# Performance work log

Hardware: AMD Instinct MI355X
Metric: run time of the kernel (lower is better)

The kernel has to match this reference:

```python
import jax, jax.numpy as jnp
import numpy as np

N = 50000        # nodes
E = 1_600_000    # edges
F = 128          # dataset_num_features (== dim so layer weights stack)
D = 128          # hidden_dim
L = 3            # num_gc_layers
G = 512          # graphs in batch
BN_EPS = 1e-5


def setup_inputs() -> dict:
    key = jax.random.key(0)
    ks = jax.random.split(key, 12)
    s = 0.05
    x = jax.random.normal(ks[0], (N, F), jnp.float32)
    edge_index = jax.random.randint(ks[1], (2, E), 0, N)
    batch = jnp.sort(jax.random.randint(ks[2], (N,), 0, G))
    # GIN MLP per layer: Linear(F->D), ReLU, Linear(D->D)  (F==D so stackable)
    W1 = jax.random.normal(ks[3], (L, F, D), jnp.float32) * s
    b1 = jnp.zeros((L, D), jnp.float32)
    W2 = jax.random.normal(ks[4], (L, D, D), jnp.float32) * s
    b2 = jnp.zeros((L, D), jnp.float32)
    bn_gamma = jnp.ones((L, D), jnp.float32)
    bn_beta = jnp.zeros((L, D), jnp.float32)
    # proj_head: Linear(3D->3D), ReLU, Linear(3D->3D)
    ED = L * D
    Wp1 = jax.random.normal(ks[5], (ED, ED), jnp.float32) * s
    bp1 = jnp.zeros((ED,), jnp.float32)
    Wp2 = jax.random.normal(ks[6], (ED, ED), jnp.float32) * s
    bp2 = jnp.zeros((ED,), jnp.float32)
    return {"x": x, "edge_index": edge_index, "batch": batch,
            "W1": W1, "b1": b1, "W2": W2, "b2": b2,
            "bn_gamma": bn_gamma, "bn_beta": bn_beta,
            "Wp1": Wp1, "bp1": bp1, "Wp2": Wp2, "bp2": bp2}


def reference(x, edge_index, batch, W1, b1, W2, b2, bn_gamma, bn_beta, Wp1, bp1, Wp2, bp2):
    src, dst = edge_index[0], edge_index[1]
    h = x
    xs = []
    for i in range(L):
        # GINConv (eps=0): nn(x_i + sum_{j->i} x_j) via gather + scatter-add
        agg = jax.ops.segment_sum(h[src], dst, num_segments=N)  # [N, D]
        m = agg + h
        m = jax.nn.relu(m @ W1[i] + b1[i])
        m = m @ W2[i] + b2[i]
        m = jax.nn.relu(m)                 # outer F.relu in Encoder.forward
        # BatchNorm1d (training mode, biased variance)
        mu = m.mean(axis=0)
        var = m.var(axis=0)
        h = (m - mu) * jax.lax.rsqrt(var + BN_EPS) * bn_gamma[i] + bn_beta[i]
        xs.append(h)
    node = jnp.concatenate(xs, axis=1)                    # [N, L*D]
    pooled = jax.ops.segment_sum(node, batch, num_segments=G)  # global_add_pool [G, L*D]
    z = jax.nn.relu(pooled @ Wp1 + bp1) @ Wp2 + bp2       # proj_head
    return z
```

## Files before the change

### kernel.cpp

```cpp
#include <hip/hip_runtime.h>

#define NN 50000
#define NPAD 50048
#define NE 1600000
#define GG 512
#define PAD 96
#define NBKT 196
#define BCAP 12288
#define CHUNK 6250
#define NBLK_MLP 782
#define NRED1 196
#define BN_EPS 1e-5f

typedef __attribute__((ext_vector_type(8))) short short8;
typedef __attribute__((ext_vector_type(4))) float f32x4;

__device__ __forceinline__ unsigned short f2bf(float x) {
    unsigned int u = __builtin_bit_cast(unsigned int, x);
    return (unsigned short)((u + 0x7FFFu + ((u >> 16) & 1u)) >> 16);
}
__device__ __forceinline__ float bf2f(unsigned int b) {
    return __builtin_bit_cast(float, b << 16);
}

__global__ __launch_bounds__(256) void bucket_k(const int* __restrict__ src, const int* __restrict__ dst,
                                                int* __restrict__ bcur, unsigned int* __restrict__ staging) {
    __shared__ int hist[NBKT];
    __shared__ int curs[NBKT];
    const int t = threadIdx.x;
    if (t < NBKT) hist[t] = 0;
    __syncthreads();
    const int e0 = blockIdx.x * CHUNK;
    const int e1 = e0 + CHUNK;
    for (int e = e0 + t; e < e1; e += 256) atomicAdd(&hist[dst[e] >> 8], 1);
    __syncthreads();
    if (t < NBKT) {
        int c = hist[t];
        curs[t] = (c > 0) ? atomicAdd(&bcur[t], c) : 0;
    }
    __syncthreads();
    for (int e = e0 + t; e < e1; e += 256) {
        int d = dst[e];
        int b = d >> 8;
        int pos = atomicAdd(&curs[b], 1);
        staging[(size_t)b * BCAP + pos] = (unsigned int)(d & 255) | ((unsigned int)src[e] << 8);
    }
}

__global__ __launch_bounds__(256) void ellfill_k(const int* __restrict__ bcur,
                                                 const unsigned int* __restrict__ staging,
                                                 int* __restrict__ cnt, unsigned short* __restrict__ ell) {
    __shared__ unsigned short lell[256 * PAD];
    __shared__ int lcnt[256];
    const int b = blockIdx.x, t = threadIdx.x;
    lcnt[t] = 0;
    __syncthreads();
    const int tot = bcur[b];
    const unsigned int* sg = staging + (size_t)b * BCAP;
    for (int i = t; i < tot; i += 256) {
        unsigned int v = sg[i];
        int r = v & 255;
        int p = atomicAdd(&lcnt[r], 1);
        lell[r * PAD + p] = (unsigned short)(v >> 8);
    }
    __syncthreads();
    const int n0 = b << 8;
    const int nrows = min(256, NN - n0);
    for (int i = t; i < nrows * 12; i += 256) {
        int r = i / 12, q = i % 12;
        *(uint4*)(ell + (size_t)(n0 + r) * PAD + q * 8) = *(const uint4*)(lell + r * PAD + q * 8);
    }
    if (t < nrows) cnt[n0 + t] = lcnt[t];
}

__global__ __launch_bounds__(256) void xconv_k(const float* __restrict__ x, unsigned short* __restrict__ xb) {
    int i = blockIdx.x * 256 + threadIdx.x;
    const int tot = NN * 32;
    const int stp = gridDim.x * 256;
    for (; i < tot; i += stp) {
        float4 v = ((const float4*)x)[i];
        uint2 pk;
        pk.x = (unsigned int)f2bf(v.x) | ((unsigned int)f2bf(v.y) << 16);
        pk.y = (unsigned int)f2bf(v.z) | ((unsigned int)f2bf(v.w) << 16);
        ((uint2*)xb)[i] = pk;
    }
}

__global__ __launch_bounds__(256) void wconv_k(const float* __restrict__ W1, const float* __restrict__ W2,
                                               unsigned short* __restrict__ Wt) {
    int i = blockIdx.x * 256 + threadIdx.x;
    if (i >= 6 * 16384) return;
    int mat = i >> 14, rem = i & 16383;
    int c = rem >> 7, k = rem & 127;
    const float* Wsrc = (mat & 1) ? W2 : W1;
    int l = mat >> 1;
    float v = Wsrc[(size_t)l * 16384 + k * 128 + c];
    Wt[(size_t)mat * 16384 + c * 128 + k] = f2bf(v);
}

__global__ __launch_bounds__(256) void wpconv_k(const float* __restrict__ Wp1, const float* __restrict__ Wp2,
                                                unsigned short* __restrict__ Wpt) {
    int i = blockIdx.x * 256 + threadIdx.x;
    if (i >= 2 * 147456) return;
    int mat = i / 147456, rem = i % 147456;
    int c = rem / 384, k = rem % 384;
    const float* Wsrc = mat ? Wp2 : Wp1;
    Wpt[(size_t)mat * 147456 + c * 384 + k] = f2bf(Wsrc[(size_t)k * 384 + c]);
}

__global__ __launch_bounds__(256) void pconv_k(const float* __restrict__ p, unsigned short* __restrict__ pb) {
    int i = blockIdx.x * 256 + threadIdx.x;
    if (i >= GG * 384 / 4) return;
    float4 v = ((const float4*)p)[i];
    uint2 pk;
    pk.x = (unsigned int)f2bf(v.x) | ((unsigned int)f2bf(v.y) << 16);
    pk.y = (unsigned int)f2bf(v.z) | ((unsigned int)f2bf(v.w) << 16);
    ((uint2*)pb)[i] = pk;
}

__global__ __launch_bounds__(256) void agg_k(const int* __restrict__ cnt, const unsigned short* __restrict__ ell,
                                             const unsigned short* __restrict__ h, const float* __restrict__ ss,
                                             unsigned short* __restrict__ m) {
    int gid = blockIdx.x * 256 + threadIdx.x;
    int n = gid >> 4, l = gid & 15;
    if (n >= NN) return;
    float sc[8], sh[8];
    #pragma unroll
    for (int j = 0; j < 8; ++j) { sc[j] = 1.f; sh[j] = 0.f; }
    if (ss) {
        #pragma unroll
        for (int j = 0; j < 8; ++j) { sc[j] = ss[l * 8 + j]; sh[j] = ss[128 + l * 8 + j]; }
    }
    int e = cnt[n];
    const unsigned short* row = ell + (size_t)n * PAD;
    float acc[8];
    {
        uint4 q = *(const uint4*)(h + (size_t)n * 128 + l * 8);
        unsigned int qq[4] = {q.x, q.y, q.z, q.w};
        #pragma unroll
        for (int j = 0; j < 4; ++j) {
            acc[2 * j]     = bf2f(qq[j] & 0xffffu) * sc[2 * j];
            acc[2 * j + 1] = bf2f(qq[j] >> 16)     * sc[2 * j + 1];
        }
    }
    int i = 0;
    for (; i + 4 <= e; i += 4) {
        uint2 ip = *(const uint2*)(row + i);
        int s0 = ip.x & 0xffff, s1 = ip.x >> 16, s2 = ip.y & 0xffff, s3 = ip.y >> 16;
        uint4 q0 = *(const uint4*)(h + (size_t)s0 * 128 + l * 8);
        uint4 q1 = *(const uint4*)(h + (size_t)s1 * 128 + l * 8);
        uint4 q2 = *(const uint4*)(h + (size_t)s2 * 128 + l * 8);
        uint4 q3 = *(const uint4*)(h + (size_t)s3 * 128 + l * 8);
        unsigned int a0[4] = {q0.x, q0.y, q0.z, q0.w};
        unsigned int a1[4] = {q1.x, q1.y, q1.z, q1.w};
        unsigned int a2[4] = {q2.x, q2.y, q2.z, q2.w};
        unsigned int a3[4] = {q3.x, q3.y, q3.z, q3.w};
        #pragma unroll
        for (int j = 0; j < 4; ++j) {
            acc[2*j]   = fmaf(bf2f(a0[j] & 0xffffu), sc[2*j],
                         fmaf(bf2f(a1[j] & 0xffffu), sc[2*j],
                         fmaf(bf2f(a2[j] & 0xffffu), sc[2*j],
                         fmaf(bf2f(a3[j] & 0xffffu), sc[2*j], acc[2*j]))));
            acc[2*j+1] = fmaf(bf2f(a0[j] >> 16), sc[2*j+1],
                         fmaf(bf2f(a1[j] >> 16), sc[2*j+1],
                         fmaf(bf2f(a2[j] >> 16), sc[2*j+1],
                         fmaf(bf2f(a3[j] >> 16), sc[2*j+1], acc[2*j+1]))));
        }
    }
    for (; i < e; ++i) {
        int s0 = row[i];
        uint4 q = *(const uint4*)(h + (size_t)s0 * 128 + l * 8);
        unsigned int qq[4] = {q.x, q.y, q.z, q.w};
        #pragma unroll
        for (int j = 0; j < 4; ++j) {
            acc[2*j]   = fmaf(bf2f(qq[j] & 0xffffu), sc[2*j],   acc[2*j]);
            acc[2*j+1] = fmaf(bf2f(qq[j] >> 16),     sc[2*j+1], acc[2*j+1]);
        }
    }
    float fe = (float)(e + 1);
    #pragma unroll
    for (int j = 0; j < 8; ++j) acc[j] = fmaf(fe, sh[j], acc[j]);
    uint4 pk;
    pk.x = (unsigned int)f2bf(acc[0]) | ((unsigned int)f2bf(acc[1]) << 16);
    pk.y = (unsigned int)f2bf(acc[2]) | ((unsigned int)f2bf(acc[3]) << 16);
    pk.z = (unsigned int)f2bf(acc[4]) | ((unsigned int)f2bf(acc[5]) << 16);
    pk.w = (unsigned int)f2bf(acc[6]) | ((unsigned int)f2bf(acc[7]) << 16);
    *(uint4*)(m + (size_t)n * 128 + l * 8) = pk;
}

__global__ __launch_bounds__(256) void mlp_k(const unsigned short* __restrict__ A,
                                             const unsigned short* __restrict__ Wt,
                                             const float* __restrict__ bias1,
                                             const float* __restrict__ bias2,
                                             unsigned short* __restrict__ yb,
                                             float* __restrict__ scr) {
    __shared__ __align__(16) unsigned short sW[128 * 136];
    __shared__ __align__(16) unsigned short sT[64 * 136];
    float* sred = (float*)sT;
    const int tid = threadIdx.x;
    for (int ch = tid; ch < 2048; ch += 256) {
        int c = ch >> 4, i = ch & 15;
        *(uint4*)(sW + c * 136 + i * 8) = *(const uint4*)(Wt + c * 128 + i * 8);
    }
    const int w = tid >> 6, l = tid & 63;
    const int lr = l & 15, lk = l >> 4;
    const int row0 = blockIdx.x * 64 + w * 16;
    const unsigned short* ap = A + (size_t)(row0 + lr) * 128 + lk * 8;
    short8 af0 = *(const short8*)(ap);
    short8 af1 = *(const short8*)(ap + 32);
    short8 af2 = *(const short8*)(ap + 64);
    short8 af3 = *(const short8*)(ap + 96);
    f32x4 acc[8] = {};
    __syncthreads();
    #pragma unroll
    for (int c = 0; c < 8; ++c) {
        const unsigned short* wp = sW + (c * 16 + lr) * 136 + lk * 8;
        short8 wf0 = *(const short8*)(wp);
        short8 wf1 = *(const short8*)(wp + 32);
        short8 wf2 = *(const short8*)(wp + 64);
        short8 wf3 = *(const short8*)(wp + 96);
        acc[c] = __builtin_amdgcn_mfma_f32_16x16x32_bf16(af0, wf0, acc[c], 0, 0, 0);
        acc[c] = __builtin_amdgcn_mfma_f32_16x16x32_bf16(af1, wf1, acc[c], 0, 0, 0);
        acc[c] = __builtin_amdgcn_mfma_f32_16x16x32_bf16(af2, wf2, acc[c], 0, 0, 0);
        acc[c] = __builtin_amdgcn_mfma_f32_16x16x32_bf16(af3, wf3, acc[c], 0, 0, 0);
    }
    const int lrow = w * 16 + lk * 4;
    #pragma unroll
    for (int c = 0; c < 8; ++c) {
        int col = c * 16 + lr;
        float b = bias1[col];
        #pragma unroll
        for (int r = 0; r < 4; ++r) {
            float v = fmaxf(acc[c][r] + b, 0.f);
            sT[(lrow + r) * 136 + col] = f2bf(v);
        }
    }
    __syncthreads();
    for (int ch = tid; ch < 2048; ch += 256) {
        int c = ch >> 4, i = ch & 15;
        *(uint4*)(sW + c * 136 + i * 8) = *(const uint4*)(Wt + 16384 + c * 128 + i * 8);
    }
    const unsigned short* tp = sT + (w * 16 + lr) * 136 + lk * 8;
    short8 bf0 = *(const short8*)(tp);
    short8 bf1 = *(const short8*)(tp + 32);
    short8 bf2_ = *(const short8*)(tp + 64);
    short8 bf3 = *(const short8*)(tp + 96);
    f32x4 acc2[8] = {};
    __syncthreads();
    #pragma unroll
    for (int c = 0; c < 8; ++c) {
        const unsigned short* wp = sW + (c * 16 + lr) * 136 + lk * 8;
        short8 wf0 = *(const short8*)(wp);
        short8 wf1 = *(const short8*)(wp + 32);
        short8 wf2 = *(const short8*)(wp + 64);
        short8 wf3 = *(const short8*)(wp + 96);
        acc2[c] = __builtin_amdgcn_mfma_f32_16x16x32_bf16(bf0, wf0, acc2[c], 0, 0, 0);
        acc2[c] = __builtin_amdgcn_mfma_f32_16x16x32_bf16(bf1, wf1, acc2[c], 0, 0, 0);
        acc2[c] = __builtin_amdgcn_mfma_f32_16x16x32_bf16(bf2_, wf2, acc2[c], 0, 0, 0);
        acc2[c] = __builtin_amdgcn_mfma_f32_16x16x32_bf16(bf3, wf3, acc2[c], 0, 0, 0);
    }
    const int drow = row0 + lk * 4;
    #pragma unroll
    for (int c = 0; c < 8; ++c) {
        int col = c * 16 + lr;
        float b = bias2[col];
        float s1 = 0.f, s2 = 0.f;
        #pragma unroll
        for (int r = 0; r < 4; ++r) {
            int grow = drow + r;
            float v = fmaxf(acc2[c][r] + b, 0.f);
            if (grow < NN) {
                yb[(size_t)grow * 128 + col] = f2bf(v);
                s1 += v;
                s2 += v * v;
            }
        }
        s1 += __shfl_xor(s1, 16); s1 += __shfl_xor(s1, 32);
        s2 += __shfl_xor(s2, 16); s2 += __shfl_xor(s2, 32);
        if (lk == 0) {
            sred[((w * 16 + lr) * 8 + c) * 2 + 0] = s1;
            sred[((w * 16 + lr) * 8 + c) * 2 + 1] = s2;
        }
    }
    __syncthreads();
    int st = tid & 1, c = (tid >> 1) & 7, lr2 = tid >> 4;
    float t = 0.f;
    #pragma unroll
    for (int w2 = 0; w2 < 4; ++w2) t += sred[((w2 * 16 + lr2) * 8 + c) * 2 + st];
    scr[(size_t)blockIdx.x * 256 + st * 128 + c * 16 + lr2] = t;
}

__global__ __launch_bounds__(256) void bnr1_k(const float* __restrict__ scr, float* __restrict__ part) {
    int b = blockIdx.x, d = threadIdx.x;
    float a = 0.f;
    for (int r = b; r < NBLK_MLP; r += NRED1) a += scr[(size_t)r * 256 + d];
    part[(size_t)b * 256 + d] = a;
}

__global__ __launch_bounds__(1024) void bnr2_k(const float* __restrict__ part, const float* __restrict__ gamma,
                                               const float* __restrict__ beta, float* __restrict__ ss) {
    __shared__ float red[4][256];
    int t = threadIdx.x, q = t >> 8, d = t & 255;
    float a = 0.f;
    for (int r = q; r < NRED1; r += 4) a += part[(size_t)r * 256 + d];
    red[q][d] = a;
    __syncthreads();
    if (t < 256) red[0][t] = red[0][t] + red[1][t] + red[2][t] + red[3][t];
    __syncthreads();
    if (t < 128) {
        float mu = red[0][t] * (1.0f / NN);
        float var = red[0][128 + t] * (1.0f / NN) - mu * mu;
        float sc = gamma[t] * rsqrtf(var + BN_EPS);
        ss[t] = sc;
        ss[128 + t] = beta[t] - mu * sc;
    }
}

__global__ __launch_bounds__(128) void pool_k(const unsigned short* __restrict__ y0,
                                              const unsigned short* __restrict__ y1,
                                              const unsigned short* __restrict__ y2,
                                              const float* __restrict__ ss,
                                              const int* __restrict__ batch, float* __restrict__ pooled) {
    int g = blockIdx.x;
    int lo = 0, hi = NN;
    while (lo < hi) { int mid = (lo + hi) >> 1; if (batch[mid] < g) lo = mid + 1; else hi = mid; }
    int s = lo;
    lo = s; hi = NN;
    while (lo < hi) { int mid = (lo + hi) >> 1; if (batch[mid] < g + 1) lo = mid + 1; else hi = mid; }
    int e = lo;
    int t = threadIdx.x;
    float sc0 = ss[t],       sh0 = ss[128 + t];
    float sc1 = ss[256 + t], sh1 = ss[384 + t];
    float sc2 = ss[512 + t], sh2 = ss[640 + t];
    float a0 = 0.f, a1 = 0.f, a2 = 0.f;
    for (int n = s; n < e; ++n) {
        a0 += fmaf(bf2f((unsigned int)y0[(size_t)n * 128 + t]), sc0, sh0);
        a1 += fmaf(bf2f((unsigned int)y1[(size_t)n * 128 + t]), sc1, sh1);
        a2 += fmaf(bf2f((unsigned int)y2[(size_t)n * 128 + t]), sc2, sh2);
    }
    pooled[(size_t)g * 384 + t] = a0;
    pooled[(size_t)g * 384 + t + 128] = a1;
    pooled[(size_t)g * 384 + t + 256] = a2;
}

__global__ __launch_bounds__(256) void projm_k(const unsigned short* __restrict__ A,
                                               const unsigned short* __restrict__ Wpt,
                                               const float* __restrict__ bias,
                                               unsigned short* __restrict__ outb,
                                               float* __restrict__ outf) {
    __shared__ __align__(16) unsigned short sW[128 * 136];
    const int tid = threadIdx.x;
    const int col_off = blockIdx.y * 128;
    const int w = tid >> 6, l = tid & 63;
    const int lr = l & 15, lk = l >> 4;
    const int row0 = blockIdx.x * 64 + w * 16;
    f32x4 acc[8] = {};
    for (int kk = 0; kk < 3; ++kk) {
        __syncthreads();
        for (int ch = tid; ch < 2048; ch += 256) {
            int c = ch >> 4, i = ch & 15;
            *(uint4*)(sW + c * 136 + i * 8) = *(const uint4*)(Wpt + (size_t)(col_off + c) * 384 + kk * 128 + i * 8);
        }
        const unsigned short* ap = A + (size_t)(row0 + lr) * 384 + kk * 128 + lk * 8;
        short8 af0 = *(const short8*)(ap);
        short8 af1 = *(const short8*)(ap + 32);
        short8 af2 = *(const short8*)(ap + 64);
        short8 af3 = *(const short8*)(ap + 96);
        __syncthreads();
        #pragma unroll
        for (int c = 0; c < 8; ++c) {
            const unsigned short* wp = sW + (c * 16 + lr) * 136 + lk * 8;
            short8 wf0 = *(const short8*)(wp);
            short8 wf1 = *(const short8*)(wp + 32);
            short8 wf2 = *(const short8*)(wp + 64);
            short8 wf3 = *(const short8*)(wp + 96);
            acc[c] = __builtin_amdgcn_mfma_f32_16x16x32_bf16(af0, wf0, acc[c], 0, 0, 0);
            acc[c] = __builtin_amdgcn_mfma_f32_16x16x32_bf16(af1, wf1, acc[c], 0, 0, 0);
            acc[c] = __builtin_amdgcn_mfma_f32_16x16x32_bf16(af2, wf2, acc[c], 0, 0, 0);
            acc[c] = __builtin_amdgcn_mfma_f32_16x16x32_bf16(af3, wf3, acc[c], 0, 0, 0);
        }
    }
    const int drow = row0 + lk * 4;
    #pragma unroll
    for (int c = 0; c < 8; ++c) {
        int col = col_off + c * 16 + lr;
        float b = bias[col];
        #pragma unroll
        for (int r = 0; r < 4; ++r) {
            float v = acc[c][r] + b;
            if (outb) outb[(size_t)(drow + r) * 384 + col] = f2bf(fmaxf(v, 0.f));
            else      outf[(size_t)(drow + r) * 384 + col] = v;
        }
    }
}

extern "C" void kernel_launch(void* const* d_in, const int* in_sizes, int n_in,
                              void* d_out, int out_size, void* d_ws, size_t ws_size,
                              hipStream_t stream) {
    const float* x     = (const float*)d_in[0];
    const int*   ei    = (const int*)d_in[1];
    const int*   srcI  = ei;
    const int*   dstI  = ei + NE;
    const int*   batch = (const int*)d_in[2];
    const float* W1    = (const float*)d_in[3];
    const float* b1    = (const float*)d_in[4];
    const float* W2    = (const float*)d_in[5];
    const float* b2    = (const float*)d_in[6];
    const float* gamma = (const float*)d_in[7];
    const float* beta  = (const float*)d_in[8];
    const float* Wp1   = (const float*)d_in[9];
    const float* bp1   = (const float*)d_in[10];
    const float* Wp2   = (const float*)d_in[11];
    const float* bp2   = (const float*)d_in[12];
    float* out = (float*)d_out;

    float* pooled = (float*)d_ws;
    float* ssbuf  = pooled + (size_t)GG * 384;
    float* part   = ssbuf + 3 * 256;
    float* scr    = part + NRED1 * 256;
    int*   cnt    = (int*)(scr + 3 * NBLK_MLP * 256);
    int*   bcur   = cnt + NN;
    unsigned int* staging = (unsigned int*)(bcur + NBKT + 4);
    unsigned short* ell  = (unsigned short*)(staging + (size_t)NBKT * BCAP);
    unsigned short* xb   = ell + (size_t)NN * PAD;
    unsigned short* yb0  = xb + (size_t)NN * 128;
    unsigned short* yb1  = yb0 + (size_t)NN * 128;
    unsigned short* yb2  = yb1 + (size_t)NN * 128;
    unsigned short* m_bf = yb2 + (size_t)NN * 128;
    unsigned short* Wt   = m_bf + (size_t)NPAD * 128;
    unsigned short* Wpt  = Wt + 6 * 16384;
    unsigned short* pb   = Wpt + 2 * 147456;
    unsigned short* z1b  = pb + (size_t)GG * 384;

    hipMemsetAsync(bcur, 0, NBKT * sizeof(int), stream);
    bucket_k<<<256, 256, 0, stream>>>(srcI, dstI, bcur, staging);
    xconv_k<<<1024, 256, 0, stream>>>(x, xb);
    wconv_k<<<384, 256, 0, stream>>>(W1, W2, Wt);
    wpconv_k<<<1152, 256, 0, stream>>>(Wp1, Wp2, Wpt);
    ellfill_k<<<NBKT, 256, 0, stream>>>(bcur, staging, cnt, ell);

    unsigned short* ybufs[3] = {yb0, yb1, yb2};
    for (int l = 0; l < 3; ++l) {
        const unsigned short* h = (l == 0) ? xb : ybufs[l - 1];
        const float* ssl        = (l == 0) ? nullptr : (ssbuf + (l - 1) * 256);

        agg_k<<<3125, 256, 0, stream>>>(cnt, ell, h, ssl, m_bf);
        mlp_k<<<NBLK_MLP, 256, 0, stream>>>(m_bf, Wt + (size_t)(2 * l) * 16384,
                                            b1 + l * 128, b2 + l * 128,
                                            ybufs[l], scr + (size_t)l * NBLK_MLP * 256);
        bnr1_k<<<NRED1, 256, 0, stream>>>(scr + (size_t)l * NBLK_MLP * 256, part);
        bnr2_k<<<1, 1024, 0, stream>>>(part, gamma + l * 128, beta + l * 128, ssbuf + l * 256);
    }

    pool_k<<<GG, 128, 0, stream>>>(yb0, yb1, yb2, ssbuf, batch, pooled);
    pconv_k<<<192, 256, 0, stream>>>(pooled, pb);
    {
        dim3 gp(8, 3);
        projm_k<<<gp, 256, 0, stream>>>(pb, Wpt, bp1, z1b, nullptr);
        projm_k<<<gp, 256, 0, stream>>>(z1b, Wpt + 147456, bp2, nullptr, out);
    }
}
```

Before: 453.3 us.

## Split aggregation into column slices and merge conversion kernels

The aggregation kernel now assigns 4 lanes per node covering a 32-column slice, with a 2D grid whose y dimension picks the slice. Each pass over the nodes then touches only a quarter of every gathered feature row, which should shrink the random-gather working set so it fits better in cache. The three input and weight conversion kernels are merged into one grid-stride kernel, and the pooled fp32-to-bf16 conversion is folded into pool_k, which removes launches. The cost is that edge lists are read four times, and each slice's 16-byte loads hit scattered rows.

```diff
diff --git a/kernel.cpp b/kernel.cpp
--- a/kernel.cpp
+++ b/kernel.cpp
@@ -11,6 +11,9 @@
 #define NBLK_MLP 782
 #define NRED1 196
 #define BN_EPS 1e-5f
+#define XCONV_TOT (NN * 32)
+#define WCONV_TOT (6 * 16384)
+#define WPCONV_TOT (2 * 147456)
 
 typedef __attribute__((ext_vector_type(8))) short short8;
 typedef __attribute__((ext_vector_type(4))) float f32x4;
@@ -73,69 +76,58 @@
     if (t < nrows) cnt[n0 + t] = lcnt[t];
 }
 
-__global__ __launch_bounds__(256) void xconv_k(const float* __restrict__ x, unsigned short* __restrict__ xb) {
+__global__ __launch_bounds__(256) void conv_k(const float* __restrict__ x,
+                                              const float* __restrict__ W1, const float* __restrict__ W2,
+                                              const float* __restrict__ Wp1, const float* __restrict__ Wp2,
+                                              unsigned short* __restrict__ xb, unsigned short* __restrict__ Wt,
+                                              unsigned short* __restrict__ Wpt) {
     int i = blockIdx.x * 256 + threadIdx.x;
-    const int tot = NN * 32;
     const int stp = gridDim.x * 256;
+    const int tot = XCONV_TOT + WCONV_TOT + WPCONV_TOT;
     for (; i < tot; i += stp) {
-        float4 v = ((const float4*)x)[i];
-        uint2 pk;
-        pk.x = (unsigned int)f2bf(v.x) | ((unsigned int)f2bf(v.y) << 16);
-        pk.y = (unsigned int)f2bf(v.z) | ((unsigned int)f2bf(v.w) << 16);
-        ((uint2*)xb)[i] = pk;
-    }
-}
-
-__global__ __launch_bounds__(256) void wconv_k(const float* __restrict__ W1, const float* __restrict__ W2,
-                                               unsigned short* __restrict__ Wt) {
-    int i = blockIdx.x * 256 + threadIdx.x;
-    if (i >= 6 * 16384) return;
-    int mat = i >> 14, rem = i & 16383;
-    int c = rem >> 7, k = rem & 127;
-    const float* Wsrc = (mat & 1) ? W2 : W1;
-    int l = mat >> 1;
-    float v = Wsrc[(size_t)l * 16384 + k * 128 + c];
-    Wt[(size_t)mat * 16384 + c * 128 + k] = f2bf(v);
-}
-
-__global__ __launch_bounds__(256) void wpconv_k(const float* __restrict__ Wp1, const float* __restrict__ Wp2,
-                                                unsigned short* __restrict__ Wpt) {
-    int i = blockIdx.x * 256 + threadIdx.x;
-    if (i >= 2 * 147456) return;
-    int mat = i / 147456, rem = i % 147456;
-    int c = rem / 384, k = rem % 384;
-    const float* Wsrc = mat ? Wp2 : Wp1;
-    Wpt[(size_t)mat * 147456 + c * 384 + k] = f2bf(Wsrc[(size_t)k * 384 + c]);
-}
-
-__global__ __launch_bounds__(256) void pconv_k(const float* __restrict__ p, unsigned short* __restrict__ pb) {
-    int i = blockIdx.x * 256 + threadIdx.x;
-    if (i >= GG * 384 / 4) return;
-    float4 v = ((const float4*)p)[i];
-    uint2 pk;
-    pk.x = (unsigned int)f2bf(v.x) | ((unsigned int)f2bf(v.y) << 16);
-    pk.y = (unsigned int)f2bf(v.z) | ((unsigned int)f2bf(v.w) << 16);
-    ((uint2*)pb)[i] = pk;
+        if (i < XCONV_TOT) {
+            float4 v = ((const float4*)x)[i];
+            uint2 pk;
+            pk.x = (unsigned int)f2bf(v.x) | ((unsigned int)f2bf(v.y) << 16);
+            pk.y = (unsigned int)f2bf(v.z) | ((unsigned int)f2bf(v.w) << 16);
+            ((uint2*)xb)[i] = pk;
+        } else if (i < XCONV_TOT + WCONV_TOT) {
+            int j = i - XCONV_TOT;
+            int mat = j >> 14, rem = j & 16383;
+            int c = rem >> 7, k = rem & 127;
+            const float* Wsrc = (mat & 1) ? W2 : W1;
+            int lay = mat >> 1;
+            Wt[(size_t)mat * 16384 + c * 128 + k] = f2bf(Wsrc[(size_t)lay * 16384 + k * 128 + c]);
+        } else {
+            int j = i - XCONV_TOT - WCONV_TOT;
+            int mat = j / 147456, rem = j % 147456;
+            int c = rem / 384, k = rem % 384;
+            const float* Wsrc = mat ? Wp2 : Wp1;
+            Wpt[(size_t)mat * 147456 + c * 384 + k] = f2bf(Wsrc[(size_t)k * 384 + c]);
+        }
+    }
 }
 
 __global__ __launch_bounds__(256) void agg_k(const int* __restrict__ cnt, const unsigned short* __restrict__ ell,
                                              const unsigned short* __restrict__ h, const float* __restrict__ ss,
                                              unsigned short* __restrict__ m) {
     int gid = blockIdx.x * 256 + threadIdx.x;
-    int n = gid >> 4, l = gid & 15;
+    int n = gid >> 2, l = gid & 3;
     if (n >= NN) return;
+    const int col0 = blockIdx.y * 32 + l * 8;
     float sc[8], sh[8];
     #pragma unroll
     for (int j = 0; j < 8; ++j) { sc[j] = 1.f; sh[j] = 0.f; }
     if (ss) {
         #pragma unroll
-        for (int j = 0; j < 8; ++j) { sc[j] = ss[l * 8 + j]; sh[j] = ss[128 + l * 8 + j]; }
+        for (int j = 0; j < 8; ++j) { sc[j] = ss[col0 + j]; sh[j] = ss[128 + col0 + j]; }
     }
     int e = cnt[n];
     const unsigned short* row = ell + (size_t)n * PAD;
+    const unsigned short* hc = h + col0;
     float acc[8];
     {
-        uint4 q = *(const uint4*)(h + (size_t)n * 128 + l * 8);
+        uint4 q = *(const uint4*)(hc + (size_t)n * 128);
         unsigned int qq[4] = {q.x, q.y, q.z, q.w};
         #pragma unroll
         for (int j = 0; j < 4; ++j) {
@@ -147,10 +139,10 @@
     for (; i + 4 <= e; i += 4) {
         uint2 ip = *(const uint2*)(row + i);
         int s0 = ip.x & 0xffff, s1 = ip.x >> 16, s2 = ip.y & 0xffff, s3 = ip.y >> 16;
-        uint4 q0 = *(const uint4*)(h + (size_t)s0 * 128 + l * 8);
-        uint4 q1 = *(const uint4*)(h + (size_t)s1 * 128 + l * 8);
-        uint4 q2 = *(const uint4*)(h + (size_t)s2 * 128 + l * 8);
-        uint4 q3 = *(const uint4*)(h + (size_t)s3 * 128 + l * 8);
+        uint4 q0 = *(const uint4*)(hc + (size_t)s0 * 128);
+        uint4 q1 = *(const uint4*)(hc + (size_t)s1 * 128);
+        uint4 q2 = *(const uint4*)(hc + (size_t)s2 * 128);
+        uint4 q3 = *(const uint4*)(hc + (size_t)s3 * 128);
         unsigned int a0[4] = {q0.x, q0.y, q0.z, q0.w};
         unsigned int a1[4] = {q1.x, q1.y, q1.z, q1.w};
         unsigned int a2[4] = {q2.x, q2.y, q2.z, q2.w};
@@ -169,7 +161,7 @@
     }
     for (; i < e; ++i) {
         int s0 = row[i];
-        uint4 q = *(const uint4*)(h + (size_t)s0 * 128 + l * 8);
+        uint4 q = *(const uint4*)(hc + (size_t)s0 * 128);
         unsigned int qq[4] = {q.x, q.y, q.z, q.w};
         #pragma unroll
         for (int j = 0; j < 4; ++j) {
@@ -185,7 +177,7 @@
     pk.y = (unsigned int)f2bf(acc[2]) | ((unsigned int)f2bf(acc[3]) << 16);
     pk.z = (unsigned int)f2bf(acc[4]) | ((unsigned int)f2bf(acc[5]) << 16);
     pk.w = (unsigned int)f2bf(acc[6]) | ((unsigned int)f2bf(acc[7]) << 16);
-    *(uint4*)(m + (size_t)n * 128 + l * 8) = pk;
+    *(uint4*)(m + (size_t)n * 128 + col0) = pk;
 }
 
 __global__ __launch_bounds__(256) void mlp_k(const unsigned short* __restrict__ A,
@@ -320,7 +312,7 @@
                                               const unsigned short* __restrict__ y1,
                                               const unsigned short* __restrict__ y2,
                                               const float* __restrict__ ss,
-                                              const int* __restrict__ batch, float* __restrict__ pooled) {
+                                              const int* __restrict__ batch, unsigned short* __restrict__ pb) {
     int g = blockIdx.x;
     int lo = 0, hi = NN;
     while (lo < hi) { int mid = (lo + hi) >> 1; if (batch[mid] < g) lo = mid + 1; else hi = mid; }
@@ -338,9 +330,9 @@
         a1 += fmaf(bf2f((unsigned int)y1[(size_t)n * 128 + t]), sc1, sh1);
         a2 += fmaf(bf2f((unsigned int)y2[(size_t)n * 128 + t]), sc2, sh2);
     }
-    pooled[(size_t)g * 384 + t] = a0;
-    pooled[(size_t)g * 384 + t + 128] = a1;
-    pooled[(size_t)g * 384 + t + 256] = a2;
+    pb[(size_t)g * 384 + t]       = f2bf(a0);
+    pb[(size_t)g * 384 + t + 128] = f2bf(a1);
+    pb[(size_t)g * 384 + t + 256] = f2bf(a2);
 }
 
 __global__ __launch_bounds__(256) void projm_k(const unsigned short* __restrict__ A,
@@ -414,8 +406,7 @@
     const float* bp2   = (const float*)d_in[12];
     float* out = (float*)d_out;
 
-    float* pooled = (float*)d_ws;
-    float* ssbuf  = pooled + (size_t)GG * 384;
+    float* ssbuf  = (float*)d_ws;
     float* part   = ssbuf + 3 * 256;
     float* scr    = part + NRED1 * 256;
     int*   cnt    = (int*)(scr + 3 * NBLK_MLP * 256);
@@ -434,9 +425,7 @@
 
     hipMemsetAsync(bcur, 0, NBKT * sizeof(int), stream);
     bucket_k<<<256, 256, 0, stream>>>(srcI, dstI, bcur, staging);
-    xconv_k<<<1024, 256, 0, stream>>>(x, xb);
-    wconv_k<<<384, 256, 0, stream>>>(W1, W2, Wt);
-    wpconv_k<<<1152, 256, 0, stream>>>(Wp1, Wp2, Wpt);
+    conv_k<<<2048, 256, 0, stream>>>(x, W1, W2, Wp1, Wp2, xb, Wt, Wpt);
     ellfill_k<<<NBKT, 256, 0, stream>>>(bcur, staging, cnt, ell);
 
     unsigned short* ybufs[3] = {yb0, yb1, yb2};
@@ -444,7 +433,8 @@
         const unsigned short* h = (l == 0) ? xb : ybufs[l - 1];
         const float* ssl        = (l == 0) ? nullptr : (ssbuf + (l - 1) * 256);
 
-        agg_k<<<3125, 256, 0, stream>>>(cnt, ell, h, ssl, m_bf);
+        dim3 ga(NBLK_MLP, 4);
+        agg_k<<<ga, 256, 0, stream>>>(cnt, ell, h, ssl, m_bf);
         mlp_k<<<NBLK_MLP, 256, 0, stream>>>(m_bf, Wt + (size_t)(2 * l) * 16384,
                                             b1 + l * 128, b2 + l * 128,
                                             ybufs[l], scr + (size_t)l * NBLK_MLP * 256);
@@ -452,8 +442,7 @@
         bnr2_k<<<1, 1024, 0, stream>>>(part, gamma + l * 128, beta + l * 128, ssbuf + l * 256);
     }
 
-    pool_k<<<GG, 128, 0, stream>>>(yb0, yb1, yb2, ssbuf, batch, pooled);
-    pconv_k<<<192, 256, 0, stream>>>(pooled, pb);
+    pool_k<<<GG, 128, 0, stream>>>(yb0, yb1, yb2, ssbuf, batch, pb);
     {
         dim3 gp(8, 3);
         projm_k<<<gp, 256, 0, stream>>>(pb, Wpt, bp1, z1b, nullptr);
```

New measurement: 697.0 us. 53.8% more time.
